# Performance work log

Measured on AMD Instinct MI355X. Metric: run time of the kernel, lower is better.

Reference implementation:

```python
import jax, jax.numpy as jnp
import numpy as np

NTYPES = 2
MAXNEI = 100
MNT = MAXNEI * NTYPES  # max_neighbor * ntypes = 200
RMIN = 0.5
RMAX = 6.0
M1 = 100   # last embedding width
M2 = 16
FH = 240   # fitting hidden width
NPHYS = 4
TFEAT = 8
B, NAT = 4, 1024


def mlp_resnet(x, Ws, bs):
    # DeepMD-style MLP: tanh layers with identity / duplicated-identity resnet
    for W, b in zip(Ws, bs):
        h = jnp.tanh(x @ W + b)
        if h.shape[-1] == x.shape[-1]:
            h = h + x
        elif h.shape[-1] == 2 * x.shape[-1]:
            h = h + jnp.concatenate([x, x], axis=-1)
        x = h
    return x


def setup_inputs() -> dict:
    key = jax.random.key(0)
    ks = jax.random.split(key, 24)
    r = jax.random.uniform(ks[0], (B, NAT, MNT), minval=0.1, maxval=7.0)
    pad = jax.random.uniform(ks[1], (B, NAT, MNT)) < 0.25
    r = jnp.where(pad, 0.0, r)
    d = jax.random.normal(ks[2], (B, NAT, MNT, 3))
    d = d / jnp.linalg.norm(d, axis=-1, keepdims=True)
    ImageDR = jnp.concatenate([r[..., None], r[..., None] * d], axis=-1).astype(jnp.float32)

    list_neigh = jax.random.randint(ks[3], (B, NAT, MNT), 0, MAXNEI)
    Imagetype_map = jax.random.randint(ks[4], (NAT,), 0, NTYPES).astype(jnp.int32)
    type_map = jnp.array([3, 14], dtype=jnp.int64)

    davg = (0.1 * jax.random.normal(ks[5], (NTYPES, MNT, 4))).astype(jnp.float32)
    dstd = (1.0 + 0.1 * jax.random.uniform(ks[6], (NTYPES, MNT, 4))).astype(jnp.float32)

    def w(k, shape):
        return (jax.random.normal(k, shape) / np.sqrt(shape[-2] if len(shape) > 1 else 1.0)).astype(jnp.float32)

    type_vector = jax.random.normal(ks[7], (NTYPES, NPHYS)).astype(jnp.float32)
    tW0 = w(ks[8], (NPHYS, TFEAT)); tb0 = jnp.zeros((TFEAT,), jnp.float32)
    eW0 = w(ks[9], (1 + TFEAT, 25)); eb0 = jnp.zeros((25,), jnp.float32)
    eW1 = w(ks[10], (25, 50));       eb1 = jnp.zeros((50,), jnp.float32)
    eW2 = w(ks[11], (50, M1));       eb2 = jnp.zeros((M1,), jnp.float32)
    fW0 = w(ks[12], (NTYPES, M2 * M1, FH)); fb0 = jnp.zeros((NTYPES, FH), jnp.float32)
    fW1 = w(ks[13], (NTYPES, FH, FH));      fb1 = jnp.zeros((NTYPES, FH), jnp.float32)
    fW2 = w(ks[14], (NTYPES, FH, FH));      fb2 = jnp.zeros((NTYPES, FH), jnp.float32)
    fWf = w(ks[15], (NTYPES, FH, 1))
    energy_shift = jnp.array([-3.2, -5.1], jnp.float32).reshape(NTYPES, 1)
    fbf = (0.01 * jax.random.normal(ks[16], (NTYPES, 1))).astype(jnp.float32) + energy_shift

    return dict(list_neigh=list_neigh, Imagetype_map=Imagetype_map, type_map=type_map,
                ImageDR=ImageDR, nghost=0, davg=davg, dstd=dstd, type_vector=type_vector,
                tW0=tW0, tb0=tb0, eW0=eW0, eb0=eb0, eW1=eW1, eb1=eb1, eW2=eW2, eb2=eb2,
                fW0=fW0, fb0=fb0, fW1=fW1, fb1=fb1, fW2=fW2, fb2=fb2, fWf=fWf, fbf=fbf)


def _forward(ImageDR, davg, dstd, type_vector, tW0, tb0, eW0, eb0, eW1, eb1, eW2, eb2,
             fW0, fb0, fW1, fb1, fW2, fb2, fWf, fbf, Imagetype_map):
    r = ImageDR[..., 0]
    r_safe = jnp.where(r > 1e-5, r, 1.0)
    inv_r = 1.0 / r_safe
    u = (r - RMIN) / (RMAX - RMIN)
    s_mid = inv_r * (u ** 3 * (-6.0 * u ** 2 + 15.0 * u - 10.0) + 1.0)
    Srij = jnp.where((r > 0) & (r < RMIN), inv_r,
                     jnp.where((r >= RMIN) & (r < RMAX), s_mid, 0.0))  # (B,N,J)
    mask = (jnp.abs(r) > 1e-5)[..., None]
    Ri = jnp.concatenate([Srij[..., None],
                          jnp.where(mask, Srij[..., None] * ImageDR[..., 1:4] * inv_r[..., None], 0.0)],
                         axis=-1)  # (B,N,J,4)
    # per-atom-type normalization
    Ri = (Ri - davg[Imagetype_map][None]) / dstd[Imagetype_map][None]

    # neighbor type feature from type-embedding net
    nt_idx = jnp.arange(MNT) // MAXNEI              # (J,) neighbor slot -> type
    tfeat = mlp_resnet(type_vector, [tW0], [tb0])   # (ntypes, TFEAT)
    nf = jnp.broadcast_to(tfeat[nt_idx][None, None], Ri.shape[:3] + (TFEAT,))
    x = jnp.concatenate([Ri[..., 0:1], nf], axis=-1)            # (B,N,J,1+TFEAT)
    G = mlp_resnet(x, [eW0, eW1, eW2], [eb0, eb1, eb2])         # (B,N,J,M1)

    xyz = jnp.einsum('bnjd,bnjm->bndm', Ri, G) / MNT            # (B,N,4,M1)
    DR = jnp.einsum('bndm,bndq->bnmq', xyz, xyz[..., :M2])      # (B,N,M1,M2)
    DR = DR.reshape(DR.shape[0], DR.shape[1], M1 * M2)

    Ei = jnp.zeros(DR.shape[:2], DR.dtype)
    for t in range(NTYPES):  # per-type fitting nets
        h = mlp_resnet(DR, [fW0[t], fW1[t], fW2[t]], [fb0[t], fb1[t], fb2[t]])
        e = (h @ fWf[t] + fbf[t])[..., 0]
        Ei = jnp.where(Imagetype_map[None, :] == t, e, Ei)
    Etot = jnp.sum(Ei, axis=1, keepdims=True)  # (B,1)
    return Etot, Ei


def reference(list_neigh, Imagetype_map, type_map, ImageDR, nghost, davg, dstd, type_vector,
              tW0, tb0, eW0, eb0, eW1, eb1, eW2, eb2,
              fW0, fb0, fW1, fb1, fW2, fb2, fWf, fbf):
    # list_neigh/type_map/nghost only participate in force computation (is_calc_f=False path)
    return _forward(ImageDR, davg, dstd, type_vector, tW0, tb0, eW0, eb0, eW1, eb1, eW2, eb2,
                    fW0, fb0, fW1, fb1, fW2, fb2, fWf, fbf, Imagetype_map)
```

## Files before the change

kernel.cpp:

```cpp
#include <hip/hip_runtime.h>
#include <hip/hip_bf16.h>

#define NATC  1024
#define BATCH 4
#define MNTC  200
#define M1C   100
#define M2C   16
#define FHC   240
#define KPAD  256
#define HSTR  264

typedef __attribute__((ext_vector_type(8))) short bf16x8;
typedef __attribute__((ext_vector_type(4))) float f32x4;

__device__ __forceinline__ float fast_tanh(float x){
    float e = __expf(2.0f * x);
    float r = __fdividef(1.0f, e + 1.0f);
    return fmaf(-2.0f, r, 1.0f);
}

__device__ __forceinline__ unsigned short f2bf(float x){
    __hip_bfloat16 h = __float2bfloat16(x);
    return *reinterpret_cast<unsigned short*>(&h);
}

__device__ __forceinline__ float bf2f(unsigned short u){
    unsigned int v = ((unsigned int)u) << 16;
    return *reinterpret_cast<float*>(&v);
}

__global__ __launch_bounds__(256) void part_kernel(const int* __restrict__ tmap,
                                                   int* __restrict__ idx,
                                                   int* __restrict__ counts){
    __shared__ int s0[256], s1[256];
    const int tid = threadIdx.x;
    int ty[4]; int c0 = 0, c1 = 0;
    #pragma unroll
    for (int r = 0; r < 4; ++r){
        ty[r] = tmap[tid*4 + r];
        if (ty[r] == 0) c0++; else c1++;
    }
    s0[tid] = c0; s1[tid] = c1;
    __syncthreads();
    for (int off = 1; off < 256; off <<= 1){
        int v0 = (tid >= off) ? s0[tid-off] : 0;
        int v1 = (tid >= off) ? s1[tid-off] : 0;
        __syncthreads();
        s0[tid] += v0; s1[tid] += v1;
        __syncthreads();
    }
    int e0 = s0[tid] - c0, e1 = s1[tid] - c1;
    #pragma unroll
    for (int r = 0; r < 4; ++r){
        int n = tid*4 + r;
        if (ty[r] == 0) idx[e0++] = n; else idx[NATC + e1++] = n;
    }
    if (tid == 255){ counts[0] = s0[255]; counts[1] = s1[255]; }
}

__global__ __launch_bounds__(256) void transp_kernel(const float* __restrict__ src,
                                                     unsigned short* __restrict__ dst,
                                                     int K, int N, int Kpad, int nkt, int nnt){
    __shared__ float tile[64][65];
    const int tid = threadIdx.x;
    int bid = blockIdx.x;
    const int t  = bid / (nkt*nnt);
    bid -= t*nkt*nnt;
    const int kt = bid / nnt;
    const int nt = bid - kt*nnt;
    const float* s = src + (size_t)t*K*N;
    unsigned short* d = dst + (size_t)t*N*Kpad;

    const int c  = tid & 63;
    const int rg = tid >> 6;
    #pragma unroll
    for (int p = 0; p < 16; ++p){
        int row = p*4 + rg;
        int gr = kt*64 + row, gc = nt*64 + c;
        tile[row][c] = (gr < K && gc < N) ? s[(size_t)gr*N + gc] : 0.0f;
    }
    __syncthreads();
    const int nn0 = tid >> 3;
    const int k8  = (tid & 7) * 8;
    #pragma unroll
    for (int p = 0; p < 2; ++p){
        int nn = p*32 + nn0;
        int gn = nt*64 + nn;
        int gk = kt*64 + k8;
        if (gn < N && gk < Kpad){
            unsigned short v[8];
            #pragma unroll
            for (int j = 0; j < 8; ++j) v[j] = f2bf(tile[k8+j][nn]);
            *(bf16x8*)(d + (size_t)gn*Kpad + gk) = *(bf16x8*)v;
        }
    }
}

__global__ __launch_bounds__(256) void prep_kernel(const float* __restrict__ tv,
                                                   const float* __restrict__ tW0,
                                                   const float* __restrict__ tb0,
                                                   const float* __restrict__ eW2,
                                                   unsigned short* __restrict__ ew2t,
                                                   float* __restrict__ tf_g){
    const int tid = threadIdx.x;
    if (tid < 16){
        int t = tid >> 3, f = tid & 7;
        float s = tb0[f];
        #pragma unroll
        for (int p = 0; p < 4; ++p) s = fmaf(tv[t*4+p], tW0[p*8+f], s);
        tf_g[tid] = fast_tanh(s) + tv[t*4 + (f & 3)];
    }
    for (int i = tid; i < 112*64; i += 256){
        int n = i >> 6, k = i & 63;
        ew2t[i] = (n < M1C && k < 50) ? f2bf(eW2[(size_t)k*M1C + n]) : (unsigned short)0;
    }
}

__global__ __launch_bounds__(256, 2) void embed_kernel(
    const float4* __restrict__ imdr,
    const float4* __restrict__ davg,
    const float4* __restrict__ dstd,
    const int*    __restrict__ tmap,
    const float*  __restrict__ tf_g,
    const float*  __restrict__ eW0,
    const float*  __restrict__ eb0,
    const float*  __restrict__ eW1,
    const float*  __restrict__ eb1,
    const float*  __restrict__ eb2,
    const unsigned short* __restrict__ ew2t,
    unsigned short* __restrict__ DRout)
{
    __shared__ unsigned short H2s[256][72];
    __shared__ float Rif[256][4];
    __shared__ float xyzp[4][4][112];
    __shared__ float xyzs[4][112];

    const int tid = threadIdx.x;
    const int a   = blockIdx.x;
    const int n   = a & (NATC - 1);
    const int itype = tmap[n];
    const int j = tid;

    if (j < MNTC){
        float4 dr = imdr[(size_t)a*MNTC + j];
        float r  = dr.x;
        float rs = (r > 1e-5f) ? r : 1.0f;
        float ir = __fdividef(1.0f, rs);
        float u  = (r - 0.5f) * (1.0f/5.5f);
        float u2 = u*u, u3 = u2*u;
        float smid = ir * (u3 * (-6.0f*u2 + 15.0f*u - 10.0f) + 1.0f);
        float S = 0.0f;
        if (r > 0.0f && r < 0.5f)       S = ir;
        else if (r >= 0.5f && r < 6.0f) S = smid;
        bool msk = fabsf(r) > 1e-5f;
        float R0 = S;
        float R1 = msk ? S * dr.y * ir : 0.0f;
        float R2 = msk ? S * dr.z * ir : 0.0f;
        float R3 = msk ? S * dr.w * ir : 0.0f;
        float4 av = davg[itype*MNTC + j];
        float4 sv = dstd[itype*MNTC + j];
        float rin0 = __fdividef(R0 - av.x, sv.x);
        float rin1 = __fdividef(R1 - av.y, sv.y);
        float rin2 = __fdividef(R2 - av.z, sv.z);
        float rin3 = __fdividef(R3 - av.w, sv.w);
        Rif[j][0] = rin0; Rif[j][1] = rin1; Rif[j][2] = rin2; Rif[j][3] = rin3;

        float xf[8];
        const int tb = (j >= 100) ? 8 : 0;
        #pragma unroll
        for (int f = 0; f < 8; ++f) xf[f] = tf_g[tb + f];

        float h1[25];
        #pragma unroll
        for (int o = 0; o < 25; ++o) h1[o] = fmaf(rin0, eW0[o], eb0[o]);
        #pragma unroll
        for (int k = 0; k < 8; ++k){
            float hv = xf[k];
            #pragma unroll
            for (int o = 0; o < 25; ++o) h1[o] = fmaf(hv, eW0[(k+1)*25 + o], h1[o]);
        }
        #pragma unroll
        for (int o = 0; o < 25; ++o) h1[o] = fast_tanh(h1[o]);

        float h2[50];
        #pragma unroll
        for (int o = 0; o < 50; ++o) h2[o] = eb1[o];
        #pragma unroll
        for (int k = 0; k < 25; ++k){
            float hv = h1[k];
            #pragma unroll
            for (int o = 0; o < 50; ++o) h2[o] = fmaf(hv, eW1[k*50 + o], h2[o]);
        }
        #pragma unroll
        for (int o = 0; o < 50; ++o) h2[o] = fast_tanh(h2[o]) + h1[o % 25];

        unsigned int* rowp = (unsigned int*)&H2s[j][0];
        #pragma unroll
        for (int c = 0; c < 25; ++c)
            rowp[c] = (unsigned int)f2bf(h2[2*c]) | ((unsigned int)f2bf(h2[2*c+1]) << 16);
        #pragma unroll
        for (int c = 25; c < 32; ++c) rowp[c] = 0u;
    } else {
        Rif[j][0] = 0.0f; Rif[j][1] = 0.0f; Rif[j][2] = 0.0f; Rif[j][3] = 0.0f;
        unsigned int* rowp = (unsigned int*)&H2s[j][0];
        #pragma unroll
        for (int c = 0; c < 32; ++c) rowp[c] = 0u;
    }
    __syncthreads();

    const int lane = tid & 63;
    const int w    = tid >> 6;
    const int lc   = lane & 15;
    const int lg   = lane >> 4;

    float bias[7];
    #pragma unroll
    for (int nt = 0; nt < 7; ++nt){
        int cg = nt*16 + lc;
        bias[nt] = (cg < M1C) ? eb2[cg] : 0.0f;
    }

    float xacc[7][4];
    #pragma unroll
    for (int nt = 0; nt < 7; ++nt)
        #pragma unroll
        for (int d = 0; d < 4; ++d) xacc[nt][d] = 0.0f;

    #pragma unroll
    for (int mi = 0; mi < 4; ++mi){
        const int mt = w + mi*4;
        const int rbase = mt*16 + lg*4;
        float4 rj[4];
        #pragma unroll
        for (int i = 0; i < 4; ++i) rj[i] = *(const float4*)&Rif[rbase + i][0];
        const unsigned short* arow = &H2s[mt*16 + lc][0];
        bf16x8 a0 = *(const bf16x8*)(arow + lg*8);
        bf16x8 a1 = *(const bf16x8*)(arow + 32 + lg*8);
        #pragma unroll
        for (int nt = 0; nt < 7; ++nt){
            const unsigned short* bp = ew2t + (size_t)(nt*16 + lc)*64 + lg*8;
            bf16x8 b0 = *(const bf16x8*)(bp);
            bf16x8 b1 = *(const bf16x8*)(bp + 32);
            f32x4 c;
            c[0] = bias[nt]; c[1] = bias[nt]; c[2] = bias[nt]; c[3] = bias[nt];
            c = __builtin_amdgcn_mfma_f32_16x16x32_bf16(a0, b0, c, 0, 0, 0);
            c = __builtin_amdgcn_mfma_f32_16x16x32_bf16(a1, b1, c, 0, 0, 0);
            const int cg = nt*16 + lc;
            const int rc = (cg >= 100) ? cg - 100 : ((cg >= 50) ? cg - 50 : cg);
            #pragma unroll
            for (int i = 0; i < 4; ++i){
                float g = fast_tanh(c[i]) + bf2f(H2s[rbase + i][rc]);
                xacc[nt][0] = fmaf(g, rj[i].x, xacc[nt][0]);
                xacc[nt][1] = fmaf(g, rj[i].y, xacc[nt][1]);
                xacc[nt][2] = fmaf(g, rj[i].z, xacc[nt][2]);
                xacc[nt][3] = fmaf(g, rj[i].w, xacc[nt][3]);
            }
        }
    }
    #pragma unroll
    for (int nt = 0; nt < 7; ++nt){
        #pragma unroll
        for (int d = 0; d < 4; ++d){
            float v = xacc[nt][d];
            v += __shfl_xor(v, 16);
            v += __shfl_xor(v, 32);
            if (lane < 16) xyzp[w][d][nt*16 + lc] = v;
        }
    }
    __syncthreads();

    for (int i = tid; i < 4*112; i += 256){
        int d = i / 112, m = i - d*112;
        xyzs[d][m] = (xyzp[0][d][m] + xyzp[1][d][m] + xyzp[2][d][m] + xyzp[3][d][m])
                     * (1.0f / (float)MNTC);
    }
    __syncthreads();

    for (int i = tid; i < M1C*M2C; i += 256){
        int m = i >> 4, q = i & 15;
        float s = 0.0f;
        #pragma unroll
        for (int d = 0; d < 4; ++d) s = fmaf(xyzs[d][m], xyzs[d][q], s);
        DRout[(size_t)a*(M1C*M2C) + i] = f2bf(s);
    }
}

__global__ __launch_bounds__(256) void fitm_kernel(
    const unsigned short* __restrict__ DRbf,
    const int*   __restrict__ idx,
    const int*   __restrict__ counts,
    const unsigned short* __restrict__ w0t,
    const unsigned short* __restrict__ w1t,
    const unsigned short* __restrict__ w2t,
    const float* __restrict__ fb0,
    const float* __restrict__ fb1,
    const float* __restrict__ fb2,
    const float* __restrict__ fWf,
    const float* __restrict__ fbf,
    float* __restrict__ out)
{
    const int bid = blockIdx.x;
    const int g = bid & 63;
    const int t = (bid >> 6) & 1;
    const int b = bid >> 7;
    const int cnt  = counts[t];
    const int base = g * 16;
    if (base >= cnt) return;
    const int na = min(16, cnt - base);

    __shared__ int ns[16];
    __shared__ unsigned short hA[16][HSTR];
    __shared__ unsigned short hB[16][HSTR];
    __shared__ float epart[4][16];

    const int tid  = threadIdx.x;
    const int lane = tid & 63;
    const int w    = tid >> 6;
    if (tid < 16) ns[tid] = idx[t*NATC + base + ((tid < na) ? tid : 0)];
    __syncthreads();

    const int lc = lane & 15;
    const int lg = lane >> 4;

    int   ncol[4];  bool act[4];  float bias0[4];
    #pragma unroll
    for (int nt = 0; nt < 4; ++nt){
        ncol[nt] = w*64 + nt*16 + lc;
        act[nt]  = (w*64 + nt*16) < FHC;
        bias0[nt] = act[nt] ? fb0[t*FHC + ncol[nt]] : 0.0f;
    }

    const unsigned short* aptr0 = DRbf + ((size_t)(b*NATC + ns[lc]))*1600 + lg*8;
    const unsigned short* bptr0[4];
    #pragma unroll
    for (int nt = 0; nt < 4; ++nt)
        bptr0[nt] = act[nt] ? (w0t + ((size_t)(t*FHC + ncol[nt]))*1600 + lg*8) : w0t;

    f32x4 acc[4];
    #pragma unroll
    for (int nt = 0; nt < 4; ++nt){
        acc[nt][0] = bias0[nt]; acc[nt][1] = bias0[nt];
        acc[nt][2] = bias0[nt]; acc[nt][3] = bias0[nt];
    }
    #pragma unroll 2
    for (int ks = 0; ks < 50; ++ks){
        bf16x8 af = *(const bf16x8*)(aptr0 + ks*32);
        #pragma unroll
        for (int nt = 0; nt < 4; ++nt){
            if (act[nt]){
                bf16x8 bfg = *(const bf16x8*)(bptr0[nt] + ks*32);
                acc[nt] = __builtin_amdgcn_mfma_f32_16x16x32_bf16(af, bfg, acc[nt], 0, 0, 0);
            }
        }
    }
    float h0r[4][4];
    #pragma unroll
    for (int nt = 0; nt < 4; ++nt){
        #pragma unroll
        for (int i = 0; i < 4; ++i){
            int row = lg*4 + i;
            if (act[nt]){
                h0r[nt][i] = fast_tanh(acc[nt][i]);
                hA[row][ncol[nt]] = f2bf(h0r[nt][i]);
            } else {
                h0r[nt][i] = 0.0f;
                hA[row][ncol[nt]] = 0;
            }
        }
    }
    __syncthreads();

    f32x4 acc1[4];
    #pragma unroll
    for (int nt = 0; nt < 4; ++nt){
        float bv = act[nt] ? fb1[t*FHC + ncol[nt]] : 0.0f;
        acc1[nt][0] = bv; acc1[nt][1] = bv; acc1[nt][2] = bv; acc1[nt][3] = bv;
    }
    const unsigned short* b1p[4];
    #pragma unroll
    for (int nt = 0; nt < 4; ++nt)
        b1p[nt] = act[nt] ? (w1t + ((size_t)(t*FHC + ncol[nt]))*KPAD + lg*8) : w1t;
    #pragma unroll
    for (int ks = 0; ks < 8; ++ks){
        bf16x8 af = *(const bf16x8*)&hA[lc][ks*32 + lg*8];
        #pragma unroll
        for (int nt = 0; nt < 4; ++nt){
            if (act[nt]){
                bf16x8 bfg = *(const bf16x8*)(b1p[nt] + ks*32);
                acc1[nt] = __builtin_amdgcn_mfma_f32_16x16x32_bf16(af, bfg, acc1[nt], 0, 0, 0);
            }
        }
    }
    float h1r[4][4];
    #pragma unroll
    for (int nt = 0; nt < 4; ++nt){
        #pragma unroll
        for (int i = 0; i < 4; ++i){
            int row = lg*4 + i;
            if (act[nt]){
                h1r[nt][i] = fast_tanh(acc1[nt][i]) + h0r[nt][i];
                hB[row][ncol[nt]] = f2bf(h1r[nt][i]);
            } else {
                h1r[nt][i] = 0.0f;
                hB[row][ncol[nt]] = 0;
            }
        }
    }
    __syncthreads();

    f32x4 acc2[4];
    #pragma unroll
    for (int nt = 0; nt < 4; ++nt){
        float bv = act[nt] ? fb2[t*FHC + ncol[nt]] : 0.0f;
        acc2[nt][0] = bv; acc2[nt][1] = bv; acc2[nt][2] = bv; acc2[nt][3] = bv;
    }
    const unsigned short* b2p[4];
    #pragma unroll
    for (int nt = 0; nt < 4; ++nt)
        b2p[nt] = act[nt] ? (w2t + ((size_t)(t*FHC + ncol[nt]))*KPAD + lg*8) : w2t;
    #pragma unroll
    for (int ks = 0; ks < 8; ++ks){
        bf16x8 af = *(const bf16x8*)&hB[lc][ks*32 + lg*8];
        #pragma unroll
        for (int nt = 0; nt < 4; ++nt){
            if (act[nt]){
                bf16x8 bfg = *(const bf16x8*)(b2p[nt] + ks*32);
                acc2[nt] = __builtin_amdgcn_mfma_f32_16x16x32_bf16(af, bfg, acc2[nt], 0, 0, 0);
            }
        }
    }

    float p0 = 0.0f, p1 = 0.0f, p2 = 0.0f, p3 = 0.0f;
    #pragma unroll
    for (int nt = 0; nt < 4; ++nt){
        if (act[nt]){
            float wfv = fWf[t*FHC + ncol[nt]];
            float h;
            h = fast_tanh(acc2[nt][0]) + h1r[nt][0]; p0 = fmaf(h, wfv, p0);
            h = fast_tanh(acc2[nt][1]) + h1r[nt][1]; p1 = fmaf(h, wfv, p1);
            h = fast_tanh(acc2[nt][2]) + h1r[nt][2]; p2 = fmaf(h, wfv, p2);
            h = fast_tanh(acc2[nt][3]) + h1r[nt][3]; p3 = fmaf(h, wfv, p3);
        }
    }
    #pragma unroll
    for (int off = 1; off < 16; off <<= 1){
        p0 += __shfl_xor(p0, off);
        p1 += __shfl_xor(p1, off);
        p2 += __shfl_xor(p2, off);
        p3 += __shfl_xor(p3, off);
    }
    if (lc == 0){
        epart[w][lg*4 + 0] = p0;
        epart[w][lg*4 + 1] = p1;
        epart[w][lg*4 + 2] = p2;
        epart[w][lg*4 + 3] = p3;
    }
    __syncthreads();
    if (tid < 16){
        float e = fbf[t] + epart[0][tid] + epart[1][tid] + epart[2][tid] + epart[3][tid];
        float ee = 0.0f;
        if (tid < na){
            out[4 + b*NATC + ns[tid]] = e;
            ee = e;
        }
        #pragma unroll
        for (int off = 8; off >= 1; off >>= 1) ee += __shfl_down(ee, off, 16);
        if (tid == 0) atomicAdd(&out[b], ee);
    }
}

extern "C" void kernel_launch(void* const* d_in, const int* in_sizes, int n_in,
                              void* d_out, int out_size, void* d_ws, size_t ws_size,
                              hipStream_t stream)
{
    (void)in_sizes; (void)n_in; (void)out_size; (void)ws_size;
    const int*   tmap = (const int*)d_in[1];
    const float* imdr = (const float*)d_in[3];
    const float* davg = (const float*)d_in[5];
    const float* dstd = (const float*)d_in[6];
    const float* tv   = (const float*)d_in[7];
    const float* tW0  = (const float*)d_in[8];
    const float* tb0  = (const float*)d_in[9];
    const float* eW0  = (const float*)d_in[10];
    const float* eb0  = (const float*)d_in[11];
    const float* eW1  = (const float*)d_in[12];
    const float* eb1  = (const float*)d_in[13];
    const float* eW2  = (const float*)d_in[14];
    const float* eb2  = (const float*)d_in[15];
    const float* fW0  = (const float*)d_in[16];
    const float* fb0  = (const float*)d_in[17];
    const float* fW1  = (const float*)d_in[18];
    const float* fb1  = (const float*)d_in[19];
    const float* fW2  = (const float*)d_in[20];
    const float* fb2  = (const float*)d_in[21];
    const float* fWf  = (const float*)d_in[22];
    const float* fbf  = (const float*)d_in[23];
    float* out = (float*)d_out;

    char* ws = (char*)d_ws;
    int*   counts = (int*)ws;
    int*   idx    = (int*)(ws + 64);
    unsigned short* DRbf = (unsigned short*)(ws + 16384);
    unsigned short* w0t  = DRbf + (size_t)BATCH*NATC*1600;
    unsigned short* w1t  = w0t + (size_t)2*FHC*1600;
    unsigned short* w2t  = w1t + (size_t)2*FHC*KPAD;
    unsigned short* ew2t = w2t + (size_t)2*FHC*KPAD;
    float* tf_g          = (float*)(ew2t + 112*64);

    hipMemsetAsync(d_out, 0, 4*sizeof(float), stream);
    part_kernel<<<1, 256, 0, stream>>>(tmap, idx, counts);
    prep_kernel<<<1, 256, 0, stream>>>(tv, tW0, tb0, eW2, ew2t, tf_g);
    transp_kernel<<<2*25*4, 256, 0, stream>>>(fW0, w0t, 1600, FHC, 1600, 25, 4);
    transp_kernel<<<2*4*4,  256, 0, stream>>>(fW1, w1t, FHC, FHC, KPAD, 4, 4);
    transp_kernel<<<2*4*4,  256, 0, stream>>>(fW2, w2t, FHC, FHC, KPAD, 4, 4);
    embed_kernel<<<BATCH*NATC, 256, 0, stream>>>(
        (const float4*)imdr, (const float4*)davg, (const float4*)dstd, tmap,
        tf_g, eW0, eb0, eW1, eb1, eb2, ew2t, DRbf);
    fitm_kernel<<<512, 256, 0, stream>>>(
        DRbf, idx, counts, w0t, w1t, w2t, fb0, fb1, fb2, fWf, fbf, out);
}
```

Measured before the change: 429.2 us.

## Move embedding layer-1 to MFMA and widen fitting kernel to 512 threads

```diff
diff --git a/kernel.cpp b/kernel.cpp
--- a/kernel.cpp
+++ b/kernel.cpp
@@ -9,6 +9,8 @@
 #define FHC   240
 #define KPAD  256
 #define HSTR  264
+#define H1STR 40
+#define H2STR 72
 
 typedef __attribute__((ext_vector_type(8))) short bf16x8;
 typedef __attribute__((ext_vector_type(4))) float f32x4;
@@ -27,6 +29,10 @@
 __device__ __forceinline__ float bf2f(unsigned short u){
     unsigned int v = ((unsigned int)u) << 16;
     return *reinterpret_cast<float*>(&v);
+}
+
+__device__ __forceinline__ unsigned int pack2(float a, float b){
+    return (unsigned int)f2bf(a) | ((unsigned int)f2bf(b) << 16);
 }
 
 __global__ __launch_bounds__(256) void part_kernel(const int* __restrict__ tmap,
@@ -99,7 +105,9 @@
 __global__ __launch_bounds__(256) void prep_kernel(const float* __restrict__ tv,
                                                    const float* __restrict__ tW0,
                                                    const float* __restrict__ tb0,
+                                                   const float* __restrict__ eW1,
                                                    const float* __restrict__ eW2,
+                                                   unsigned short* __restrict__ ew1t,
                                                    unsigned short* __restrict__ ew2t,
                                                    float* __restrict__ tf_g){
     const int tid = threadIdx.x;
@@ -113,6 +121,10 @@
     for (int i = tid; i < 112*64; i += 256){
         int n = i >> 6, k = i & 63;
         ew2t[i] = (n < M1C && k < 50) ? f2bf(eW2[(size_t)k*M1C + n]) : (unsigned short)0;
+    }
+    for (int i = tid; i < 64*32; i += 256){
+        int n = i >> 5, k = i & 31;
+        ew1t[i] = (n < 50 && k < 25) ? f2bf(eW1[(size_t)k*50 + n]) : (unsigned short)0;
     }
 }
 
@@ -124,87 +136,75 @@
     const float*  __restrict__ tf_g,
     const float*  __restrict__ eW0,
     const float*  __restrict__ eb0,
-    const float*  __restrict__ eW1,
     const float*  __restrict__ eb1,
     const float*  __restrict__ eb2,
+    const unsigned short* __restrict__ ew1t,
     const unsigned short* __restrict__ ew2t,
     unsigned short* __restrict__ DRout)
 {
-    __shared__ unsigned short H2s[256][72];
-    __shared__ float Rif[256][4];
-    __shared__ float xyzp[4][4][112];
-    __shared__ float xyzs[4][112];
+    __shared__ __align__(16) float Rif[256][4];
+    __shared__ __align__(16) unsigned short H1s[256][H1STR];
+    __shared__ __align__(16) unsigned short H2s[256][H2STR];
 
     const int tid = threadIdx.x;
     const int a   = blockIdx.x;
-    const int n   = a & (NATC - 1);
-    const int itype = tmap[n];
+    const int n0  = a & (NATC - 1);
+    const int itype = tmap[n0];
     const int j = tid;
 
-    if (j < MNTC){
-        float4 dr = imdr[(size_t)a*MNTC + j];
-        float r  = dr.x;
-        float rs = (r > 1e-5f) ? r : 1.0f;
-        float ir = __fdividef(1.0f, rs);
-        float u  = (r - 0.5f) * (1.0f/5.5f);
-        float u2 = u*u, u3 = u2*u;
-        float smid = ir * (u3 * (-6.0f*u2 + 15.0f*u - 10.0f) + 1.0f);
-        float S = 0.0f;
-        if (r > 0.0f && r < 0.5f)       S = ir;
-        else if (r >= 0.5f && r < 6.0f) S = smid;
-        bool msk = fabsf(r) > 1e-5f;
-        float R0 = S;
-        float R1 = msk ? S * dr.y * ir : 0.0f;
-        float R2 = msk ? S * dr.z * ir : 0.0f;
-        float R3 = msk ? S * dr.w * ir : 0.0f;
-        float4 av = davg[itype*MNTC + j];
-        float4 sv = dstd[itype*MNTC + j];
-        float rin0 = __fdividef(R0 - av.x, sv.x);
-        float rin1 = __fdividef(R1 - av.y, sv.y);
-        float rin2 = __fdividef(R2 - av.z, sv.z);
-        float rin3 = __fdividef(R3 - av.w, sv.w);
-        Rif[j][0] = rin0; Rif[j][1] = rin1; Rif[j][2] = rin2; Rif[j][3] = rin3;
-
-        float xf[8];
-        const int tb = (j >= 100) ? 8 : 0;
-        #pragma unroll
-        for (int f = 0; f < 8; ++f) xf[f] = tf_g[tb + f];
-
-        float h1[25];
-        #pragma unroll
-        for (int o = 0; o < 25; ++o) h1[o] = fmaf(rin0, eW0[o], eb0[o]);
-        #pragma unroll
-        for (int k = 0; k < 8; ++k){
-            float hv = xf[k];
-            #pragma unroll
-            for (int o = 0; o < 25; ++o) h1[o] = fmaf(hv, eW0[(k+1)*25 + o], h1[o]);
-        }
-        #pragma unroll
-        for (int o = 0; o < 25; ++o) h1[o] = fast_tanh(h1[o]);
-
-        float h2[50];
-        #pragma unroll
-        for (int o = 0; o < 50; ++o) h2[o] = eb1[o];
-        #pragma unroll
-        for (int k = 0; k < 25; ++k){
-            float hv = h1[k];
-            #pragma unroll
-            for (int o = 0; o < 50; ++o) h2[o] = fmaf(hv, eW1[k*50 + o], h2[o]);
-        }
-        #pragma unroll
-        for (int o = 0; o < 50; ++o) h2[o] = fast_tanh(h2[o]) + h1[o % 25];
-
-        unsigned int* rowp = (unsigned int*)&H2s[j][0];
-        #pragma unroll
-        for (int c = 0; c < 25; ++c)
-            rowp[c] = (unsigned int)f2bf(h2[2*c]) | ((unsigned int)f2bf(h2[2*c+1]) << 16);
-        #pragma unroll
-        for (int c = 25; c < 32; ++c) rowp[c] = 0u;
-    } else {
-        Rif[j][0] = 0.0f; Rif[j][1] = 0.0f; Rif[j][2] = 0.0f; Rif[j][3] = 0.0f;
-        unsigned int* rowp = (unsigned int*)&H2s[j][0];
-        #pragma unroll
-        for (int c = 0; c < 32; ++c) rowp[c] = 0u;
+    {
+        unsigned int* rowp = (unsigned int*)&H1s[j][0];
+        if (j < MNTC){
+            float4 dr = imdr[(size_t)a*MNTC + j];
+            float r  = dr.x;
+            float rs = (r > 1e-5f) ? r : 1.0f;
+            float ir = __fdividef(1.0f, rs);
+            float u  = (r - 0.5f) * (1.0f/5.5f);
+            float u2 = u*u, u3 = u2*u;
+            float smid = ir * (u3 * (-6.0f*u2 + 15.0f*u - 10.0f) + 1.0f);
+            float S = 0.0f;
+            if (r > 0.0f && r < 0.5f)       S = ir;
+            else if (r >= 0.5f && r < 6.0f) S = smid;
+            bool msk = fabsf(r) > 1e-5f;
+            float R0 = S;
+            float R1 = msk ? S * dr.y * ir : 0.0f;
+            float R2 = msk ? S * dr.z * ir : 0.0f;
+            float R3 = msk ? S * dr.w * ir : 0.0f;
+            float4 av = davg[itype*MNTC + j];
+            float4 sv = dstd[itype*MNTC + j];
+            float rin0 = __fdividef(R0 - av.x, sv.x);
+            float rin1 = __fdividef(R1 - av.y, sv.y);
+            float rin2 = __fdividef(R2 - av.z, sv.z);
+            float rin3 = __fdividef(R3 - av.w, sv.w);
+            Rif[j][0] = rin0; Rif[j][1] = rin1; Rif[j][2] = rin2; Rif[j][3] = rin3;
+
+            float xf[8];
+            const int tb = (j >= 100) ? 8 : 0;
+            #pragma unroll
+            for (int f = 0; f < 8; ++f) xf[f] = tf_g[tb + f];
+
+            float h1[25];
+            #pragma unroll
+            for (int o = 0; o < 25; ++o) h1[o] = fmaf(rin0, eW0[o], eb0[o]);
+            #pragma unroll
+            for (int k = 0; k < 8; ++k){
+                float hv = xf[k];
+                #pragma unroll
+                for (int o = 0; o < 25; ++o) h1[o] = fmaf(hv, eW0[(k+1)*25 + o], h1[o]);
+            }
+            #pragma unroll
+            for (int o = 0; o < 25; ++o) h1[o] = fast_tanh(h1[o]);
+
+            #pragma unroll
+            for (int c = 0; c < 12; ++c) rowp[c] = pack2(h1[2*c], h1[2*c+1]);
+            rowp[12] = (unsigned int)f2bf(h1[24]);
+            #pragma unroll
+            for (int c = 13; c < 20; ++c) rowp[c] = 0u;
+        } else {
+            Rif[j][0] = 0.0f; Rif[j][1] = 0.0f; Rif[j][2] = 0.0f; Rif[j][3] = 0.0f;
+            #pragma unroll
+            for (int c = 0; c < 20; ++c) rowp[c] = 0u;
+        }
     }
     __syncthreads();
 
@@ -212,6 +212,35 @@
     const int w    = tid >> 6;
     const int lc   = lane & 15;
     const int lg   = lane >> 4;
+
+    #pragma unroll
+    for (int mi = 0; mi < 4; ++mi){
+        const int mt = w + mi*4;
+        bf16x8 af = *(const bf16x8*)&H1s[mt*16 + lc][lg*8];
+        const int rbase = mt*16 + lg*4;
+        #pragma unroll
+        for (int nt = 0; nt < 4; ++nt){
+            const int n = nt*16 + lc;
+            const bool live = (n < 50);
+            float bv = live ? eb1[n] : 0.0f;
+            f32x4 c;
+            c[0] = bv; c[1] = bv; c[2] = bv; c[3] = bv;
+            bf16x8 bfr = *(const bf16x8*)(ew1t + n*32 + lg*8);
+            c = __builtin_amdgcn_mfma_f32_16x16x32_bf16(af, bfr, c, 0, 0, 0);
+            const int rc = n % 25;
+            #pragma unroll
+            for (int i = 0; i < 4; ++i){
+                const int row = rbase + i;
+                unsigned short v = 0;
+                if (live) v = f2bf(fast_tanh(c[i]) + bf2f(H1s[row][rc]));
+                H2s[row][n] = v;
+            }
+        }
+    }
+    __syncthreads();
+
+    float* xyzp = (float*)&H1s[0][0];
+    float* xyzs = xyzp + 4*4*112;
 
     float bias[7];
     #pragma unroll
@@ -264,15 +293,16 @@
             float v = xacc[nt][d];
             v += __shfl_xor(v, 16);
             v += __shfl_xor(v, 32);
-            if (lane < 16) xyzp[w][d][nt*16 + lc] = v;
+            if (lane < 16) xyzp[((w*4 + d)*112) + nt*16 + lc] = v;
         }
     }
     __syncthreads();
 
     for (int i = tid; i < 4*112; i += 256){
         int d = i / 112, m = i - d*112;
-        xyzs[d][m] = (xyzp[0][d][m] + xyzp[1][d][m] + xyzp[2][d][m] + xyzp[3][d][m])
-                     * (1.0f / (float)MNTC);
+        xyzs[d*112 + m] = (xyzp[(0*4+d)*112 + m] + xyzp[(1*4+d)*112 + m] +
+                           xyzp[(2*4+d)*112 + m] + xyzp[(3*4+d)*112 + m])
+                          * (1.0f / (float)MNTC);
     }
     __syncthreads();
 
@@ -280,12 +310,12 @@
         int m = i >> 4, q = i & 15;
         float s = 0.0f;
         #pragma unroll
-        for (int d = 0; d < 4; ++d) s = fmaf(xyzs[d][m], xyzs[d][q], s);
+        for (int d = 0; d < 4; ++d) s = fmaf(xyzs[d*112 + m], xyzs[d*112 + q], s);
         DRout[(size_t)a*(M1C*M2C) + i] = f2bf(s);
     }
 }
 
-__global__ __launch_bounds__(256) void fitm_kernel(
+__global__ __launch_bounds__(512) void fitm_kernel(
     const unsigned short* __restrict__ DRbf,
     const int*   __restrict__ idx,
     const int*   __restrict__ counts,
@@ -309,9 +339,9 @@
     const int na = min(16, cnt - base);
 
     __shared__ int ns[16];
-    __shared__ unsigned short hA[16][HSTR];
-    __shared__ unsigned short hB[16][HSTR];
-    __shared__ float epart[4][16];
+    __shared__ __align__(16) unsigned short hA[16][HSTR];
+    __shared__ __align__(16) unsigned short hB[16][HSTR];
+    __shared__ float epart[8][16];
 
     const int tid  = threadIdx.x;
     const int lane = tid & 63;
@@ -322,40 +352,40 @@
     const int lc = lane & 15;
     const int lg = lane >> 4;
 
-    int   ncol[4];  bool act[4];  float bias0[4];
-    #pragma unroll
-    for (int nt = 0; nt < 4; ++nt){
-        ncol[nt] = w*64 + nt*16 + lc;
-        act[nt]  = (w*64 + nt*16) < FHC;
+    int   ncol[2];  bool act[2];  float bias0[2];
+    #pragma unroll
+    for (int nt = 0; nt < 2; ++nt){
+        ncol[nt] = w*32 + nt*16 + lc;
+        act[nt]  = (w*32 + nt*16) < FHC;
         bias0[nt] = act[nt] ? fb0[t*FHC + ncol[nt]] : 0.0f;
     }
 
     const unsigned short* aptr0 = DRbf + ((size_t)(b*NATC + ns[lc]))*1600 + lg*8;
-    const unsigned short* bptr0[4];
-    #pragma unroll
-    for (int nt = 0; nt < 4; ++nt)
+    const unsigned short* bptr0[2];
+    #pragma unroll
+    for (int nt = 0; nt < 2; ++nt)
         bptr0[nt] = act[nt] ? (w0t + ((size_t)(t*FHC + ncol[nt]))*1600 + lg*8) : w0t;
 
-    f32x4 acc[4];
-    #pragma unroll
-    for (int nt = 0; nt < 4; ++nt){
+    f32x4 acc[2];
+    #pragma unroll
+    for (int nt = 0; nt < 2; ++nt){
         acc[nt][0] = bias0[nt]; acc[nt][1] = bias0[nt];
         acc[nt][2] = bias0[nt]; acc[nt][3] = bias0[nt];
     }
-    #pragma unroll 2
+    #pragma unroll 4
     for (int ks = 0; ks < 50; ++ks){
         bf16x8 af = *(const bf16x8*)(aptr0 + ks*32);
         #pragma unroll
-        for (int nt = 0; nt < 4; ++nt){
+        for (int nt = 0; nt < 2; ++nt){
             if (act[nt]){
                 bf16x8 bfg = *(const bf16x8*)(bptr0[nt] + ks*32);
                 acc[nt] = __builtin_amdgcn_mfma_f32_16x16x32_bf16(af, bfg, acc[nt], 0, 0, 0);
             }
         }
     }
-    float h0r[4][4];
-    #pragma unroll
-    for (int nt = 0; nt < 4; ++nt){
+    float h0r[2][4];
+    #pragma unroll
+    for (int nt = 0; nt < 2; ++nt){
         #pragma unroll
         for (int i = 0; i < 4; ++i){
             int row = lg*4 + i;
@@ -370,30 +400,30 @@
     }
     __syncthreads();
 
-    f32x4 acc1[4];
-    #pragma unroll
-    for (int nt = 0; nt < 4; ++nt){
+    f32x4 acc1[2];
+    #pragma unroll
+    for (int nt = 0; nt < 2; ++nt){
         float bv = act[nt] ? fb1[t*FHC + ncol[nt]] : 0.0f;
         acc1[nt][0] = bv; acc1[nt][1] = bv; acc1[nt][2] = bv; acc1[nt][3] = bv;
     }
-    const unsigned short* b1p[4];
-    #pragma unroll
-    for (int nt = 0; nt < 4; ++nt)
+    const unsigned short* b1p[2];
+    #pragma unroll
+    for (int nt = 0; nt < 2; ++nt)
         b1p[nt] = act[nt] ? (w1t + ((size_t)(t*FHC + ncol[nt]))*KPAD + lg*8) : w1t;
     #pragma unroll
     for (int ks = 0; ks < 8; ++ks){
         bf16x8 af = *(const bf16x8*)&hA[lc][ks*32 + lg*8];
         #pragma unroll
-        for (int nt = 0; nt < 4; ++nt){
+        for (int nt = 0; nt < 2; ++nt){
             if (act[nt]){
                 bf16x8 bfg = *(const bf16x8*)(b1p[nt] + ks*32);
                 acc1[nt] = __builtin_amdgcn_mfma_f32_16x16x32_bf16(af, bfg, acc1[nt], 0, 0, 0);
             }
         }
     }
-    float h1r[4][4];
-    #pragma unroll
-    for (int nt = 0; nt < 4; ++nt){
+    float h1r[2][4];
+    #pragma unroll
+    for (int nt = 0; nt < 2; ++nt){
         #pragma unroll
         for (int i = 0; i < 4; ++i){
             int row = lg*4 + i;
@@ -408,21 +438,21 @@
     }
     __syncthreads();
 
-    f32x4 acc2[4];
-    #pragma unroll
-    for (int nt = 0; nt < 4; ++nt){
+    f32x4 acc2[2];
+    #pragma unroll
+    for (int nt = 0; nt < 2; ++nt){
         float bv = act[nt] ? fb2[t*FHC + ncol[nt]] : 0.0f;
         acc2[nt][0] = bv; acc2[nt][1] = bv; acc2[nt][2] = bv; acc2[nt][3] = bv;
     }
-    const unsigned short* b2p[4];
-    #pragma unroll
-    for (int nt = 0; nt < 4; ++nt)
+    const unsigned short* b2p[2];
+    #pragma unroll
+    for (int nt = 0; nt < 2; ++nt)
         b2p[nt] = act[nt] ? (w2t + ((size_t)(t*FHC + ncol[nt]))*KPAD + lg*8) : w2t;
     #pragma unroll
     for (int ks = 0; ks < 8; ++ks){
         bf16x8 af = *(const bf16x8*)&hB[lc][ks*32 + lg*8];
         #pragma unroll
-        for (int nt = 0; nt < 4; ++nt){
+        for (int nt = 0; nt < 2; ++nt){
             if (act[nt]){
                 bf16x8 bfg = *(const bf16x8*)(b2p[nt] + ks*32);
                 acc2[nt] = __builtin_amdgcn_mfma_f32_16x16x32_bf16(af, bfg, acc2[nt], 0, 0, 0);
@@ -432,7 +462,7 @@
 
     float p0 = 0.0f, p1 = 0.0f, p2 = 0.0f, p3 = 0.0f;
     #pragma unroll
-    for (int nt = 0; nt < 4; ++nt){
+    for (int nt = 0; nt < 2; ++nt){
         if (act[nt]){
             float wfv = fWf[t*FHC + ncol[nt]];
             float h;
@@ -457,7 +487,9 @@
     }
     __syncthreads();
     if (tid < 16){
-        float e = fbf[t] + epart[0][tid] + epart[1][tid] + epart[2][tid] + epart[3][tid];
+        float e = fbf[t];
+        #pragma unroll
+        for (int ww = 0; ww < 8; ++ww) e += epart[ww][tid];
         float ee = 0.0f;
         if (tid < na){
             out[4 + b*NATC + ns[tid]] = e;
@@ -505,17 +537,18 @@
     unsigned short* w1t  = w0t + (size_t)2*FHC*1600;
     unsigned short* w2t  = w1t + (size_t)2*FHC*KPAD;
     unsigned short* ew2t = w2t + (size_t)2*FHC*KPAD;
-    float* tf_g          = (float*)(ew2t + 112*64);
+    unsigned short* ew1t = ew2t + 112*64;
+    float* tf_g          = (float*)(ew1t + 64*32);
 
     hipMemsetAsync(d_out, 0, 4*sizeof(float), stream);
     part_kernel<<<1, 256, 0, stream>>>(tmap, idx, counts);
-    prep_kernel<<<1, 256, 0, stream>>>(tv, tW0, tb0, eW2, ew2t, tf_g);
+    prep_kernel<<<1, 256, 0, stream>>>(tv, tW0, tb0, eW1, eW2, ew1t, ew2t, tf_g);
     transp_kernel<<<2*25*4, 256, 0, stream>>>(fW0, w0t, 1600, FHC, 1600, 25, 4);
     transp_kernel<<<2*4*4,  256, 0, stream>>>(fW1, w1t, FHC, FHC, KPAD, 4, 4);
     transp_kernel<<<2*4*4,  256, 0, stream>>>(fW2, w2t, FHC, FHC, KPAD, 4, 4);
     embed_kernel<<<BATCH*NATC, 256, 0, stream>>>(
         (const float4*)imdr, (const float4*)davg, (const float4*)dstd, tmap,
-        tf_g, eW0, eb0, eW1, eb1, eb2, ew2t, DRbf);
-    fitm_kernel<<<512, 256, 0, stream>>>(
+        tf_g, eW0, eb0, eb1, eb2, ew1t, ew2t, DRbf);
+    fitm_kernel<<<512, 512, 0, stream>>>(
         DRbf, idx, counts, w0t, w1t, w2t, fb0, fb1, fb2, fWf, fbf, out);
 }
```

Measured after the change: 413.9 us. -3.6%, faster.
